# Performance work log

Hardware: AMD Instinct MI355X
Metric: run time of the kernel (lower is better)

Reference implementation:

```python
import jax, jax.numpy as jnp
import numpy as np

EPS = 1e-8  # PoissonNLLLoss default eps

def _pair_loss(inp, tgt):
    # Poisson NLL (log_input=False, full=True), summed over detector dim D,
    # for every (hypothesis i, measurement j) pair WITHOUT materializing [N,M,D]:
    # loss_ij = sum_d inp[i,d] - sum_d tgt[j,d]*log(inp[i,d]+eps) + sum_d stirling(tgt[j,d])
    log_in = jnp.log(inp + EPS)                         # [N,D]
    s_in = jnp.sum(inp, axis=1)                         # [N]
    cross = jnp.einsum('id,jd->ij', log_in, tgt)        # [N,M]
    t_safe = jnp.where(tgt > 1, tgt, 1.0)
    stirling = jnp.where(
        tgt > 1,
        tgt * jnp.log(t_safe) - tgt + 0.5 * jnp.log(2.0 * jnp.pi * t_safe),
        0.0,
    )
    s_st = jnp.sum(stirling, axis=1)                    # [M]
    return s_in[:, None] - cross + s_st[None, :]        # [N,M]

def setup_inputs() -> dict:
    key = jax.random.key(0)
    k1, k2 = jax.random.split(key)
    N, M, D = 10000, 10000, 180
    # photon-count-like positive values; scale so target>1 hits Stirling branch
    inp = jax.random.uniform(k1, (N, D), dtype=jnp.float32) * 100.0
    tgt = jax.random.uniform(k2, (M, D), dtype=jnp.float32) * 100.0
    return {"input": inp, "target": tgt}

def reference(input, target):
    L = _pair_loss(input, target)          # [N,M]
    loss_v = jnp.min(L, axis=1)            # [N]
    match = jnp.argmin(L, axis=1)          # [N] int
    loss = jnp.mean(loss_v)
    return (loss, match)
```

## Files before the change

### kernel.cpp

```cpp
#include <hip/hip_runtime.h>
#include <math.h>

#define EPSF 1e-8f

typedef _Float16 f16x8 __attribute__((ext_vector_type(8)));
typedef float f32x4 __attribute__((ext_vector_type(4)));

#define GLOAD_LDS16(g, l)                                                      \
  __builtin_amdgcn_global_load_lds(                                            \
      (const __attribute__((address_space(1))) unsigned int*)(g),              \
      (__attribute__((address_space(3))) unsigned int*)(l), 16, 0, 0)

#define WAITV(n) asm volatile("s_waitcnt vmcnt(" #n ")" ::: "memory")
#define BAR() __builtin_amdgcn_s_barrier()

__device__ __forceinline__ unsigned int ord_from_float(float f) {
  unsigned int u = __float_as_uint(f);
  return (u & 0x80000000u) ? ~u : (u | 0x80000000u);
}

__device__ __forceinline__ float float_from_ord(unsigned int o) {
  return (o & 0x80000000u) ? __uint_as_float(o & 0x7fffffffu)
                           : __uint_as_float(~o);
}

__device__ __forceinline__ unsigned long long shfl_xor_u64(unsigned long long x, int m) {
  int lo = __shfl_xor((int)(unsigned int)(x & 0xffffffffull), m, 64);
  int hi = __shfl_xor((int)(unsigned int)(x >> 32), m, 64);
  return ((unsigned long long)(unsigned int)hi << 32) | (unsigned int)lo;
}

__global__ __launch_bounds__(64) void prep_A_kernel(
    const float* __restrict__ inp, _Float16* __restrict__ Acat,
    float* __restrict__ s_in, unsigned long long* __restrict__ packed,
    int N, int D, int DP) {
  int r = blockIdx.x;
  const size_t base = (size_t)r * (3 * DP);
  float s = 0.f;
  for (int d = threadIdx.x; d < DP; d += 64) {
    float lg = 0.f;
    if (r < N && d < D) {
      float x = inp[(size_t)r * D + d];
      s += x;
      lg = logf(x + EPSF);
    }
    _Float16 h = (_Float16)lg;
    _Float16 l = (_Float16)(lg - (float)h);
    Acat[base + d] = h;
    Acat[base + DP + d] = h;
    Acat[base + 2 * DP + d] = l;
  }
  #pragma unroll
  for (int m = 1; m < 64; m <<= 1) s += __shfl_xor(s, m, 64);
  if (threadIdx.x == 0 && r < N) {
    s_in[r] = s;
    packed[r] = ~0ull;
  }
}

__global__ __launch_bounds__(64) void prep_B_kernel(
    const float* __restrict__ tgt, _Float16* __restrict__ Bcat,
    float* __restrict__ s_st, int M, int D, int DP) {
  int r = blockIdx.x;
  const size_t base = (size_t)r * (3 * DP);
  float s = 0.f;
  for (int d = threadIdx.x; d < DP; d += 64) {
    float x = 0.f;
    if (r < M && d < D) {
      x = tgt[(size_t)r * D + d];
      if (x > 1.0f)
        s += x * logf(x) - x + 0.5f * logf(6.283185307179586f * x);
    }
    _Float16 h = (_Float16)x;
    _Float16 l = (_Float16)(x - (float)h);
    Bcat[base + d] = h;
    Bcat[base + DP + d] = l;
    Bcat[base + 2 * DP + d] = h;
  }
  #pragma unroll
  for (int m = 1; m < 64; m <<= 1) s += __shfl_xor(s, m, 64);
  if (threadIdx.x == 0 && r < M) s_st[r] = s;
}

#define BT 256
#define BUFH 8192

__global__ __launch_bounds__(512, 2) void mfma_pair_min_kernel(
    const _Float16* __restrict__ Acat, const _Float16* __restrict__ Bcat,
    const float* __restrict__ s_st, unsigned long long* __restrict__ packed,
    int N, int M, int KP, int gx) {
  extern __shared__ __align__(16) _Float16 smem[];
  _Float16* const AshB = smem;
  _Float16* const BshB = smem + 4 * BUFH;

  const int t = threadIdx.x;
  const int lane = t & 63;
  const int wid = t >> 6;
  const int wr = wid >> 2;
  const int wc = wid & 3;

  const int nwg = gridDim.x;
  const int q8 = nwg >> 3;
  const int xcd = blockIdx.x & 7;
  const int i8 = blockIdx.x >> 3;
  int brow, bcol;
  if (q8 % gx == 0) {
    int bh = q8 / gx;
    brow = xcd * bh + i8 % bh;
    bcol = i8 / bh;
  } else {
    int wg = xcd * q8 + i8;
    brow = wg / gx;
    bcol = wg % gx;
  }
  const int row0 = brow * BT;
  const int col0 = bcol * BT;

  f32x4 acc[8][4] = {};

  const int srow = lane >> 2;
  const int gs = (lane & 3) ^ ((lane >> 3) & 3);
  const _Float16* const aSrc = Acat + (size_t)(row0 + wid * 32 + srow) * KP + gs * 8;
  const _Float16* const bSrc = Bcat + (size_t)(col0 + wid * 32 + srow) * KP + gs * 8;
  _Float16* const lA = AshB + wid * 1024;
  _Float16* const lB = BshB + wid * 1024;

#define STAGE(buf, step)                                                       \
  do {                                                                         \
    const int so_ = (step) * 32;                                               \
    GLOAD_LDS16(aSrc + so_, lA + (buf) * BUFH);                                \
    GLOAD_LDS16(aSrc + so_ + 16 * KP, lA + (buf) * BUFH + 512);                \
    GLOAD_LDS16(bSrc + so_, lB + (buf) * BUFH);                                \
    GLOAD_LDS16(bSrc + so_ + 16 * KP, lB + (buf) * BUFH + 512);                \
  } while (0)

  const int rl = lane & 15;
  const int qq = lane >> 4;
  const int sa = qq ^ ((rl >> 1) & 3);

#define COMPUTE(buf)                                                           \
  do {                                                                         \
    const int bofs_ = (buf) * BUFH;                                            \
    f16x8 af[8], bf[4];                                                        \
    _Pragma("unroll")                                                          \
    for (int m = 0; m < 8; ++m)                                                \
      af[m] = *(const f16x8*)(&AshB[bofs_ + (wr * 128 + m * 16 + rl) * 32 + sa * 8]); \
    _Pragma("unroll")                                                          \
    for (int n = 0; n < 4; ++n)                                                \
      bf[n] = *(const f16x8*)(&BshB[bofs_ + (wc * 64 + n * 16 + rl) * 32 + sa * 8]); \
    __builtin_amdgcn_s_setprio(1);                                             \
    _Pragma("unroll")                                                          \
    for (int m = 0; m < 8; ++m)                                                \
      _Pragma("unroll")                                                        \
      for (int n = 0; n < 4; ++n)                                              \
        acc[m][n] = __builtin_amdgcn_mfma_f32_16x16x32_f16(af[m], bf[n],       \
                                                           acc[m][n], 0, 0, 0); \
    __builtin_amdgcn_s_setprio(0);                                             \
  } while (0)

  const int NT = KP >> 5;

  STAGE(0, 0);
  STAGE(1, 1);
  STAGE(2, 2);
  WAITV(8);
  BAR();

  int kt = 0;
  for (; kt < NT - 3; ++kt) {
    STAGE((kt + 3) & 3, kt + 3);
    COMPUTE(kt & 3);
    WAITV(8);
    BAR();
  }
  COMPUTE(kt & 3);
  WAITV(4);
  BAR();
  ++kt;
  COMPUTE(kt & 3);
  WAITV(0);
  BAR();
  ++kt;
  COMPUTE(kt & 3);

#undef STAGE
#undef COMPUTE

  float stv[4];
  #pragma unroll
  for (int n = 0; n < 4; ++n) {
    int gj = col0 + wc * 64 + n * 16 + rl;
    stv[n] = (gj < M) ? s_st[gj] : __builtin_inff();
  }
  #pragma unroll
  for (int m = 0; m < 8; ++m) {
    #pragma unroll
    for (int g = 0; g < 4; ++g) {
      int grow = row0 + wr * 128 + m * 16 + qq * 4 + g;
      unsigned long long bst = ~0ull;
      #pragma unroll
      for (int n = 0; n < 4; ++n) {
        int gj = col0 + wc * 64 + n * 16 + rl;
        float val = stv[n] - acc[m][n][g];
        unsigned long long p =
            ((unsigned long long)ord_from_float(val) << 32) | (unsigned int)gj;
        if (p < bst) bst = p;
      }
      #pragma unroll
      for (int mm = 1; mm < 16; mm <<= 1) {
        unsigned long long o = shfl_xor_u64(bst, mm);
        if (o < bst) bst = o;
      }
      if (rl == 0 && grow < N) atomicMin(&packed[grow], bst);
    }
  }
}


__global__ __launch_bounds__(256) void finalize_kernel(
    const unsigned long long* __restrict__ packed,
    const float* __restrict__ s_in, float* __restrict__ out, int N) {
  __shared__ double sh[256];
  double s = 0.0;
  for (int i = threadIdx.x; i < N; i += 256) {
    unsigned long long p = packed[i];
    float val = float_from_ord((unsigned int)(p >> 32));
    out[1 + i] = (float)(unsigned int)(p & 0xffffffffull);
    s += (double)(s_in[i] + val);
  }
  sh[threadIdx.x] = s;
  __syncthreads();
  for (int off = 128; off > 0; off >>= 1) {
    if (threadIdx.x < off) sh[threadIdx.x] += sh[threadIdx.x + off];
    __syncthreads();
  }
  if (threadIdx.x == 0) out[0] = (float)(sh[0] / N);
}

extern "C" void kernel_launch(void* const* d_in, const int* in_sizes, int n_in,
                              void* d_out, int out_size, void* d_ws, size_t ws_size,
                              hipStream_t stream) {
  const float* inp = (const float*)d_in[0];
  const float* tgt = (const float*)d_in[1];
  float* out = (float*)d_out;

  int N = out_size - 1;
  int D = in_sizes[0] / N;
  int M = in_sizes[1] / D;

  int Npad = ((N + BT - 1) / BT) * BT;
  int Mpad = ((M + BT - 1) / BT) * BT;
  int DP = ((D + 31) / 32) * 32;
  int KP = 3 * DP;

  char* ws = (char*)d_ws;
  size_t off = 0;
  float* s_in = (float*)(ws + off); off += (size_t)N * 4;
  float* s_st = (float*)(ws + off); off += (size_t)M * 4;
  off = (off + 15) & ~(size_t)15;
  unsigned long long* packed = (unsigned long long*)(ws + off); off += (size_t)N * 8;
  off = (off + 15) & ~(size_t)15;
  _Float16* Acat = (_Float16*)(ws + off); off += (size_t)Npad * KP * 2;
  _Float16* Bcat = (_Float16*)(ws + off); off += (size_t)Mpad * KP * 2;

  prep_A_kernel<<<Npad, 64, 0, stream>>>(inp, Acat, s_in, packed, N, D, DP);
  prep_B_kernel<<<Mpad, 64, 0, stream>>>(tgt, Bcat, s_st, M, D, DP);

  const int ldsBytes = 8 * BUFH * 2;
  hipFuncSetAttribute((const void*)mfma_pair_min_kernel,
                      hipFuncAttributeMaxDynamicSharedMemorySize, ldsBytes);

  int gx = Mpad / BT, gy = Npad / BT;
  mfma_pair_min_kernel<<<gx * gy, 512, ldsBytes, stream>>>(Acat, Bcat, s_st,
                                                           packed, N, M, KP, gx);

  finalize_kernel<<<1, 256, 0, stream>>>(packed, s_in, out, N);
}
```

Before: 213.7 us.

## Restructure MFMA main loop into ping-pong register-fragment pipeline over 64-wide K tiles

Rewrites the GEMM main loop so each 64-wide K tile is split into two K halves and two M halves. LDS fragment loads for the next quarter-tile are interleaved with the MFMAs of the current one through double-buffered register fragments, and global-to-LDS stages are spread across the sub-steps. The K dimension is padded to an odd number of 64-element tiles, with zero fill in the prep kernels, to fit the unrolled two-tile loop. This is meant to hide LDS read latency behind MFMA work, at the cost of more barriers per tile, a few extra padded K elements, and a fragile hand-written schedule.

```diff
diff --git a/kernel.cpp b/kernel.cpp
--- a/kernel.cpp
+++ b/kernel.cpp
@@ -33,9 +33,9 @@
 __global__ __launch_bounds__(64) void prep_A_kernel(
     const float* __restrict__ inp, _Float16* __restrict__ Acat,
     float* __restrict__ s_in, unsigned long long* __restrict__ packed,
-    int N, int D, int DP) {
+    int N, int D, int DP, int KPA) {
   int r = blockIdx.x;
-  const size_t base = (size_t)r * (3 * DP);
+  _Float16* row = Acat + (size_t)r * KPA;
   float s = 0.f;
   for (int d = threadIdx.x; d < DP; d += 64) {
     float lg = 0.f;
@@ -46,10 +46,11 @@
     }
     _Float16 h = (_Float16)lg;
     _Float16 l = (_Float16)(lg - (float)h);
-    Acat[base + d] = h;
-    Acat[base + DP + d] = h;
-    Acat[base + 2 * DP + d] = l;
-  }
+    row[d] = h;
+    row[DP + d] = h;
+    row[2 * DP + d] = l;
+  }
+  for (int d = threadIdx.x; d < KPA - 3 * DP; d += 64) row[3 * DP + d] = (_Float16)0.f;
   #pragma unroll
   for (int m = 1; m < 64; m <<= 1) s += __shfl_xor(s, m, 64);
   if (threadIdx.x == 0 && r < N) {
@@ -60,9 +61,9 @@
 
 __global__ __launch_bounds__(64) void prep_B_kernel(
     const float* __restrict__ tgt, _Float16* __restrict__ Bcat,
-    float* __restrict__ s_st, int M, int D, int DP) {
+    float* __restrict__ s_st, int M, int D, int DP, int KPA) {
   int r = blockIdx.x;
-  const size_t base = (size_t)r * (3 * DP);
+  _Float16* row = Bcat + (size_t)r * KPA;
   float s = 0.f;
   for (int d = threadIdx.x; d < DP; d += 64) {
     float x = 0.f;
@@ -73,26 +74,24 @@
     }
     _Float16 h = (_Float16)x;
     _Float16 l = (_Float16)(x - (float)h);
-    Bcat[base + d] = h;
-    Bcat[base + DP + d] = l;
-    Bcat[base + 2 * DP + d] = h;
-  }
+    row[d] = h;
+    row[DP + d] = l;
+    row[2 * DP + d] = h;
+  }
+  for (int d = threadIdx.x; d < KPA - 3 * DP; d += 64) row[3 * DP + d] = (_Float16)0.f;
   #pragma unroll
   for (int m = 1; m < 64; m <<= 1) s += __shfl_xor(s, m, 64);
   if (threadIdx.x == 0 && r < M) s_st[r] = s;
 }
 
 #define BT 256
-#define BUFH 8192
+#define UNITH 8192
 
 __global__ __launch_bounds__(512, 2) void mfma_pair_min_kernel(
     const _Float16* __restrict__ Acat, const _Float16* __restrict__ Bcat,
     const float* __restrict__ s_st, unsigned long long* __restrict__ packed,
-    int N, int M, int KP, int gx) {
+    int N, int M, int KPA, int gx) {
   extern __shared__ __align__(16) _Float16 smem[];
-  _Float16* const AshB = smem;
-  _Float16* const BshB = smem + 4 * BUFH;
-
   const int t = threadIdx.x;
   const int lane = t & 63;
   const int wid = t >> 6;
@@ -116,75 +115,92 @@
   const int row0 = brow * BT;
   const int col0 = bcol * BT;
 
-  f32x4 acc[8][4] = {};
-
   const int srow = lane >> 2;
   const int gs = (lane & 3) ^ ((lane >> 3) & 3);
-  const _Float16* const aSrc = Acat + (size_t)(row0 + wid * 32 + srow) * KP + gs * 8;
-  const _Float16* const bSrc = Bcat + (size_t)(col0 + wid * 32 + srow) * KP + gs * 8;
-  _Float16* const lA = AshB + wid * 1024;
-  _Float16* const lB = BshB + wid * 1024;
-
-#define STAGE(buf, step)                                                       \
-  do {                                                                         \
-    const int so_ = (step) * 32;                                               \
-    GLOAD_LDS16(aSrc + so_, lA + (buf) * BUFH);                                \
-    GLOAD_LDS16(aSrc + so_ + 16 * KP, lA + (buf) * BUFH + 512);                \
-    GLOAD_LDS16(bSrc + so_, lB + (buf) * BUFH);                                \
-    GLOAD_LDS16(bSrc + so_ + 16 * KP, lB + (buf) * BUFH + 512);                \
+  const _Float16* pA0 = Acat + (size_t)(row0 + wid * 32 + srow) * KPA + gs * 8;
+  const _Float16* pA1 = pA0 + (size_t)16 * KPA;
+  const _Float16* pB0 = Bcat + (size_t)(col0 + wid * 32 + srow) * KPA + gs * 8;
+  const _Float16* pB1 = pB0 + (size_t)16 * KPA;
+  _Float16* const ldst = smem + wid * 1024;
+
+#define STG(b_, isB_, kh_, tofs_)                                              \
+  do {                                                                         \
+    const _Float16* s0_ = ((isB_) ? pB0 : pA0) + (tofs_) * 64 + (kh_) * 32;    \
+    const _Float16* s1_ = ((isB_) ? pB1 : pA1) + (tofs_) * 64 + (kh_) * 32;    \
+    _Float16* d_ = ldst + ((((b_) << 2) | ((isB_) << 1) | (kh_)) * UNITH);     \
+    GLOAD_LDS16(s0_, d_);                                                      \
+    GLOAD_LDS16(s1_, d_ + 512);                                                \
   } while (0)
 
   const int rl = lane & 15;
-  const int qq = lane >> 4;
-  const int sa = qq ^ ((rl >> 1) & 3);
-
-#define COMPUTE(buf)                                                           \
-  do {                                                                         \
-    const int bofs_ = (buf) * BUFH;                                            \
-    f16x8 af[8], bf[4];                                                        \
-    _Pragma("unroll")                                                          \
-    for (int m = 0; m < 8; ++m)                                                \
-      af[m] = *(const f16x8*)(&AshB[bofs_ + (wr * 128 + m * 16 + rl) * 32 + sa * 8]); \
-    _Pragma("unroll")                                                          \
-    for (int n = 0; n < 4; ++n)                                                \
-      bf[n] = *(const f16x8*)(&BshB[bofs_ + (wc * 64 + n * 16 + rl) * 32 + sa * 8]); \
+  const int q = lane >> 4;
+  const int sa = q ^ ((rl >> 1) & 3);
+
+#define LDA4(dst_, b_, kh_, mh_)                                               \
+  do {                                                                         \
+    const _Float16* p_ = smem + ((((b_) << 2) | (kh_)) * UNITH);               \
+    _Pragma("unroll") for (int mm_ = 0; mm_ < 4; ++mm_)                        \
+        dst_[mm_] = *(const f16x8*)(p_ + (wr * 128 + (mh_) * 64 + mm_ * 16 + rl) * 32 + sa * 8); \
+  } while (0)
+
+#define LDB4(dst_, b_, kh_)                                                    \
+  do {                                                                         \
+    const _Float16* p_ = smem + ((((b_) << 2) | 2 | (kh_)) * UNITH);           \
+    _Pragma("unroll") for (int nn_ = 0; nn_ < 4; ++nn_)                        \
+        dst_[nn_] = *(const f16x8*)(p_ + (wc * 64 + nn_ * 16 + rl) * 32 + sa * 8); \
+  } while (0)
+
+  f32x4 acc[8][4] = {};
+  f16x8 afA[4], afB[4], bfA[4], bfB[4];
+
+#define MMQ(af_, bf_, mh_)                                                     \
+  do {                                                                         \
     __builtin_amdgcn_s_setprio(1);                                             \
-    _Pragma("unroll")                                                          \
-    for (int m = 0; m < 8; ++m)                                                \
-      _Pragma("unroll")                                                        \
-      for (int n = 0; n < 4; ++n)                                              \
-        acc[m][n] = __builtin_amdgcn_mfma_f32_16x16x32_f16(af[m], bf[n],       \
-                                                           acc[m][n], 0, 0, 0); \
+    _Pragma("unroll") for (int mm_ = 0; mm_ < 4; ++mm_)                        \
+        _Pragma("unroll") for (int nn_ = 0; nn_ < 4; ++nn_)                    \
+            acc[(mh_) * 4 + mm_][nn_] = __builtin_amdgcn_mfma_f32_16x16x32_f16(\
+                af_[mm_], bf_[nn_], acc[(mh_) * 4 + mm_][nn_], 0, 0, 0);       \
     __builtin_amdgcn_s_setprio(0);                                             \
   } while (0)
 
-  const int NT = KP >> 5;
-
-  STAGE(0, 0);
-  STAGE(1, 1);
-  STAGE(2, 2);
-  WAITV(8);
+  STG(0, 0, 0, 0); STG(0, 1, 0, 0); STG(0, 0, 1, 0); STG(0, 1, 1, 0);
+  STG(1, 0, 0, 1); STG(1, 1, 0, 1); STG(1, 1, 1, 1);
+  WAITV(10);
   BAR();
-
-  int kt = 0;
-  for (; kt < NT - 3; ++kt) {
-    STAGE((kt + 3) & 3, kt + 3);
-    COMPUTE(kt & 3);
-    WAITV(8);
-    BAR();
-  }
-  COMPUTE(kt & 3);
-  WAITV(4);
-  BAR();
-  ++kt;
-  COMPUTE(kt & 3);
-  WAITV(0);
-  BAR();
-  ++kt;
-  COMPUTE(kt & 3);
-
-#undef STAGE
-#undef COMPUTE
+  LDA4(afA, 0, 0, 0);
+  LDB4(bfA, 0, 0);
+
+  const int LITERS = ((KPA >> 6) - 3) >> 1;
+  for (int i = 0; i < LITERS; ++i) {
+    LDA4(afB, 0, 0, 1); STG(1, 0, 1, 1);                  BAR(); MMQ(afA, bfA, 0); WAITV(8); BAR();
+    LDA4(afA, 0, 1, 0); LDB4(bfB, 0, 1); STG(0, 0, 0, 2); BAR(); MMQ(afB, bfA, 1);           BAR();
+    LDA4(afB, 0, 1, 1); STG(0, 1, 0, 2);                  BAR(); MMQ(afA, bfB, 0); WAITV(8); BAR();
+    LDA4(afA, 1, 0, 0); LDB4(bfA, 1, 0); STG(0, 1, 1, 2); BAR(); MMQ(afB, bfB, 1);           BAR();
+    LDA4(afB, 1, 0, 1); STG(0, 0, 1, 2);                  BAR(); MMQ(afA, bfA, 0); WAITV(8); BAR();
+    LDA4(afA, 1, 1, 0); LDB4(bfB, 1, 1); STG(1, 1, 0, 3); BAR(); MMQ(afB, bfA, 1);           BAR();
+    LDA4(afB, 1, 1, 1); STG(1, 0, 0, 3);                  BAR(); MMQ(afA, bfB, 0); WAITV(8); BAR();
+    LDA4(afA, 0, 0, 0); LDB4(bfA, 0, 0); STG(1, 1, 1, 3); BAR(); MMQ(afB, bfB, 1);           BAR();
+    pA0 += 128; pA1 += 128; pB0 += 128; pB1 += 128;
+  }
+
+  LDA4(afB, 0, 0, 1); STG(1, 0, 1, 1);                  BAR(); MMQ(afA, bfA, 0); WAITV(8); BAR();
+  LDA4(afA, 0, 1, 0); LDB4(bfB, 0, 1); STG(0, 0, 0, 2); BAR(); MMQ(afB, bfA, 1);           BAR();
+  LDA4(afB, 0, 1, 1); STG(0, 1, 0, 2);                  BAR(); MMQ(afA, bfB, 0); WAITV(8); BAR();
+  LDA4(afA, 1, 0, 0); LDB4(bfA, 1, 0); STG(0, 1, 1, 2); BAR(); MMQ(afB, bfB, 1);           BAR();
+  LDA4(afB, 1, 0, 1); STG(0, 0, 1, 2);                  BAR(); MMQ(afA, bfA, 0); WAITV(8); BAR();
+  LDA4(afA, 1, 1, 0); LDB4(bfB, 1, 1);                  BAR(); MMQ(afB, bfA, 1);           BAR();
+  LDA4(afB, 1, 1, 1);                                   BAR(); MMQ(afA, bfB, 0); WAITV(4); BAR();
+  LDA4(afA, 0, 0, 0); LDB4(bfA, 0, 0);                  BAR(); MMQ(afB, bfB, 1);           BAR();
+
+  LDA4(afB, 0, 0, 1);                                   BAR(); MMQ(afA, bfA, 0); WAITV(0); BAR();
+  LDA4(afA, 0, 1, 0); LDB4(bfB, 0, 1);                  BAR(); MMQ(afB, bfA, 1);           BAR();
+  LDA4(afB, 0, 1, 1);                                   BAR(); MMQ(afA, bfB, 0);           BAR();
+                                                        BAR(); MMQ(afB, bfB, 1);
+
+#undef STG
+#undef LDA4
+#undef LDB4
+#undef MMQ
 
   float stv[4];
   #pragma unroll
@@ -196,7 +212,7 @@
   for (int m = 0; m < 8; ++m) {
     #pragma unroll
     for (int g = 0; g < 4; ++g) {
-      int grow = row0 + wr * 128 + m * 16 + qq * 4 + g;
+      int grow = row0 + wr * 128 + m * 16 + q * 4 + g;
       unsigned long long bst = ~0ull;
       #pragma unroll
       for (int n = 0; n < 4; ++n) {
@@ -251,7 +267,9 @@
   int Npad = ((N + BT - 1) / BT) * BT;
   int Mpad = ((M + BT - 1) / BT) * BT;
   int DP = ((D + 31) / 32) * 32;
-  int KP = 3 * DP;
+  int TT = (3 * DP + 63) / 64;
+  if ((TT & 1) == 0) ++TT;
+  int KPA = TT * 64;
 
   char* ws = (char*)d_ws;
   size_t off = 0;
@@ -260,19 +278,19 @@
   off = (off + 15) & ~(size_t)15;
   unsigned long long* packed = (unsigned long long*)(ws + off); off += (size_t)N * 8;
   off = (off + 15) & ~(size_t)15;
-  _Float16* Acat = (_Float16*)(ws + off); off += (size_t)Npad * KP * 2;
-  _Float16* Bcat = (_Float16*)(ws + off); off += (size_t)Mpad * KP * 2;
-
-  prep_A_kernel<<<Npad, 64, 0, stream>>>(inp, Acat, s_in, packed, N, D, DP);
-  prep_B_kernel<<<Mpad, 64, 0, stream>>>(tgt, Bcat, s_st, M, D, DP);
-
-  const int ldsBytes = 8 * BUFH * 2;
+  _Float16* Acat = (_Float16*)(ws + off); off += (size_t)Npad * KPA * 2;
+  _Float16* Bcat = (_Float16*)(ws + off); off += (size_t)Mpad * KPA * 2;
+
+  prep_A_kernel<<<Npad, 64, 0, stream>>>(inp, Acat, s_in, packed, N, D, DP, KPA);
+  prep_B_kernel<<<Mpad, 64, 0, stream>>>(tgt, Bcat, s_st, M, D, DP, KPA);
+
+  const int ldsBytes = 8 * UNITH * 2;
   hipFuncSetAttribute((const void*)mfma_pair_min_kernel,
                       hipFuncAttributeMaxDynamicSharedMemorySize, ldsBytes);
 
   int gx = Mpad / BT, gy = Npad / BT;
   mfma_pair_min_kernel<<<gx * gy, 512, ldsBytes, stream>>>(Acat, Bcat, s_st,
-                                                           packed, N, M, KP, gx);
+                                                           packed, N, M, KPA, gx);
 
   finalize_kernel<<<1, 256, 0, stream>>>(packed, s_in, out, N);
 }
```

After: 213.1 us. No clear change (-0.3%).

## Replace global atomicMin with per-tile partial minima and parallel reduction

Applied to the files above, without the earlier changes.

The main kernel now reduces the row minima across its four column-warps in shared memory and writes one partial result per (column tile, row) to a buffer, instead of issuing global 64-bit atomicMin calls. A new multi-block reduce kernel takes the min over column tiles and accumulates the mean through a fixed-point atomic add. This replaces the single-block finalize. The two prep kernels are merged into one launch. The trade is an extra partial buffer plus two extra small launches and a memset, in exchange for removing atomic contention and the serial finalize.

```diff
diff --git a/kernel.cpp b/kernel.cpp
--- a/kernel.cpp
+++ b/kernel.cpp
@@ -30,56 +30,52 @@
   return ((unsigned long long)(unsigned int)hi << 32) | (unsigned int)lo;
 }
 
-__global__ __launch_bounds__(64) void prep_A_kernel(
-    const float* __restrict__ inp, _Float16* __restrict__ Acat,
-    float* __restrict__ s_in, unsigned long long* __restrict__ packed,
-    int N, int D, int DP) {
-  int r = blockIdx.x;
-  const size_t base = (size_t)r * (3 * DP);
-  float s = 0.f;
-  for (int d = threadIdx.x; d < DP; d += 64) {
-    float lg = 0.f;
-    if (r < N && d < D) {
-      float x = inp[(size_t)r * D + d];
-      s += x;
-      lg = logf(x + EPSF);
-    }
-    _Float16 h = (_Float16)lg;
-    _Float16 l = (_Float16)(lg - (float)h);
-    Acat[base + d] = h;
-    Acat[base + DP + d] = h;
-    Acat[base + 2 * DP + d] = l;
-  }
-  #pragma unroll
-  for (int m = 1; m < 64; m <<= 1) s += __shfl_xor(s, m, 64);
-  if (threadIdx.x == 0 && r < N) {
-    s_in[r] = s;
-    packed[r] = ~0ull;
-  }
-}
-
-__global__ __launch_bounds__(64) void prep_B_kernel(
-    const float* __restrict__ tgt, _Float16* __restrict__ Bcat,
-    float* __restrict__ s_st, int M, int D, int DP) {
-  int r = blockIdx.x;
-  const size_t base = (size_t)r * (3 * DP);
-  float s = 0.f;
-  for (int d = threadIdx.x; d < DP; d += 64) {
-    float x = 0.f;
-    if (r < M && d < D) {
-      x = tgt[(size_t)r * D + d];
-      if (x > 1.0f)
-        s += x * logf(x) - x + 0.5f * logf(6.283185307179586f * x);
-    }
-    _Float16 h = (_Float16)x;
-    _Float16 l = (_Float16)(x - (float)h);
-    Bcat[base + d] = h;
-    Bcat[base + DP + d] = l;
-    Bcat[base + 2 * DP + d] = h;
-  }
-  #pragma unroll
-  for (int m = 1; m < 64; m <<= 1) s += __shfl_xor(s, m, 64);
-  if (threadIdx.x == 0 && r < M) s_st[r] = s;
+__global__ __launch_bounds__(64) void prep_kernel(
+    const float* __restrict__ inp, const float* __restrict__ tgt,
+    _Float16* __restrict__ Acat, _Float16* __restrict__ Bcat,
+    float* __restrict__ s_in, float* __restrict__ s_st,
+    int N, int M, int Npad, int Mpad, int D, int DP, int KPA) {
+  const int r = blockIdx.x;
+  if (r < Npad) {
+    _Float16* row = Acat + (size_t)r * KPA;
+    float s = 0.f;
+    for (int d = threadIdx.x; d < DP; d += 64) {
+      float lg = 0.f;
+      if (r < N && d < D) {
+        float x = inp[(size_t)r * D + d];
+        s += x;
+        lg = logf(x + EPSF);
+      }
+      _Float16 h = (_Float16)lg;
+      _Float16 l = (_Float16)(lg - (float)h);
+      row[d] = h;
+      row[DP + d] = h;
+      row[2 * DP + d] = l;
+    }
+    #pragma unroll
+    for (int m = 1; m < 64; m <<= 1) s += __shfl_xor(s, m, 64);
+    if (threadIdx.x == 0 && r < N) s_in[r] = s;
+  }
+  if (r < Mpad) {
+    _Float16* row = Bcat + (size_t)r * KPA;
+    float s = 0.f;
+    for (int d = threadIdx.x; d < DP; d += 64) {
+      float x = 0.f;
+      if (r < M && d < D) {
+        x = tgt[(size_t)r * D + d];
+        if (x > 1.0f)
+          s += x * logf(x) - x + 0.5f * logf(6.283185307179586f * x);
+      }
+      _Float16 h = (_Float16)x;
+      _Float16 l = (_Float16)(x - (float)h);
+      row[d] = h;
+      row[DP + d] = l;
+      row[2 * DP + d] = h;
+    }
+    #pragma unroll
+    for (int m = 1; m < 64; m <<= 1) s += __shfl_xor(s, m, 64);
+    if (threadIdx.x == 0 && r < M) s_st[r] = s;
+  }
 }
 
 #define BT 256
@@ -87,8 +83,8 @@
 
 __global__ __launch_bounds__(512, 2) void mfma_pair_min_kernel(
     const _Float16* __restrict__ Acat, const _Float16* __restrict__ Bcat,
-    const float* __restrict__ s_st, unsigned long long* __restrict__ packed,
-    int N, int M, int KP, int gx) {
+    const float* __restrict__ s_st, unsigned long long* __restrict__ packed2,
+    int N, int M, int KPA, int gx, int Npad) {
   extern __shared__ __align__(16) _Float16 smem[];
   _Float16* const AshB = smem;
   _Float16* const BshB = smem + 4 * BUFH;
@@ -120,18 +116,18 @@
 
   const int srow = lane >> 2;
   const int gs = (lane & 3) ^ ((lane >> 3) & 3);
-  const _Float16* const aSrc = Acat + (size_t)(row0 + wid * 32 + srow) * KP + gs * 8;
-  const _Float16* const bSrc = Bcat + (size_t)(col0 + wid * 32 + srow) * KP + gs * 8;
-  _Float16* const lA = AshB + wid * 1024;
-  _Float16* const lB = BshB + wid * 1024;
+  const _Float16* a0 = Acat + (size_t)(row0 + wid * 32 + srow) * KPA + gs * 8;
+  const _Float16* a1 = a0 + (size_t)16 * KPA;
+  const _Float16* b0 = Bcat + (size_t)(col0 + wid * 32 + srow) * KPA + gs * 8;
+  const _Float16* b1 = b0 + (size_t)16 * KPA;
 
 #define STAGE(buf, step)                                                       \
   do {                                                                         \
     const int so_ = (step) * 32;                                               \
-    GLOAD_LDS16(aSrc + so_, lA + (buf) * BUFH);                                \
-    GLOAD_LDS16(aSrc + so_ + 16 * KP, lA + (buf) * BUFH + 512);                \
-    GLOAD_LDS16(bSrc + so_, lB + (buf) * BUFH);                                \
-    GLOAD_LDS16(bSrc + so_ + 16 * KP, lB + (buf) * BUFH + 512);                \
+    GLOAD_LDS16(a0 + so_, AshB + wid * 1024 + (buf) * BUFH);                   \
+    GLOAD_LDS16(a1 + so_, AshB + wid * 1024 + (buf) * BUFH + 512);             \
+    GLOAD_LDS16(b0 + so_, BshB + wid * 1024 + (buf) * BUFH);                   \
+    GLOAD_LDS16(b1 + so_, BshB + wid * 1024 + (buf) * BUFH + 512);             \
   } while (0)
 
   const int rl = lane & 15;
@@ -158,7 +154,7 @@
     __builtin_amdgcn_s_setprio(0);                                             \
   } while (0)
 
-  const int NT = KP >> 5;
+  const int NT = KPA >> 5;
 
   STAGE(0, 0);
   STAGE(1, 1);
@@ -192,11 +188,14 @@
     int gj = col0 + wc * 64 + n * 16 + rl;
     stv[n] = (gj < M) ? s_st[gj] : __builtin_inff();
   }
+
+  __syncthreads();
+  unsigned long long* red = (unsigned long long*)smem;
+
   #pragma unroll
   for (int m = 0; m < 8; ++m) {
     #pragma unroll
     for (int g = 0; g < 4; ++g) {
-      int grow = row0 + wr * 128 + m * 16 + qq * 4 + g;
       unsigned long long bst = ~0ull;
       #pragma unroll
       for (int n = 0; n < 4; ++n) {
@@ -211,30 +210,60 @@
         unsigned long long o = shfl_xor_u64(bst, mm);
         if (o < bst) bst = o;
       }
-      if (rl == 0 && grow < N) atomicMin(&packed[grow], bst);
-    }
-  }
-}
-
-
-__global__ __launch_bounds__(256) void finalize_kernel(
-    const unsigned long long* __restrict__ packed,
-    const float* __restrict__ s_in, float* __restrict__ out, int N) {
+      if (rl == 0)
+        red[wc * 256 + wr * 128 + m * 16 + qq * 4 + g] = bst;
+    }
+  }
+  __syncthreads();
+
+  if (t < 256) {
+    int grow = row0 + t;
+    if (grow < N) {
+      unsigned long long b0 = red[t];
+      unsigned long long b1 = red[256 + t];
+      unsigned long long b2 = red[512 + t];
+      unsigned long long b3 = red[768 + t];
+      unsigned long long best = b0 < b1 ? b0 : b1;
+      if (b2 < best) best = b2;
+      if (b3 < best) best = b3;
+      packed2[(size_t)bcol * Npad + grow] = best;
+    }
+  }
+}
+
+__global__ __launch_bounds__(256) void reduce_kernel(
+    const unsigned long long* __restrict__ packed2,
+    const float* __restrict__ s_in, float* __restrict__ out,
+    unsigned long long* __restrict__ sumbuf, int N, int Npad, int gx) {
+  int i = blockIdx.x * 256 + threadIdx.x;
+  double local = 0.0;
+  if (i < N) {
+    unsigned long long best = ~0ull;
+    for (int c = 0; c < gx; ++c) {
+      unsigned long long p = packed2[(size_t)c * Npad + i];
+      if (p < best) best = p;
+    }
+    out[1 + i] = (float)(unsigned int)(best & 0xffffffffull);
+    float val = float_from_ord((unsigned int)(best >> 32));
+    local = (double)(s_in[i] + val);
+  }
   __shared__ double sh[256];
-  double s = 0.0;
-  for (int i = threadIdx.x; i < N; i += 256) {
-    unsigned long long p = packed[i];
-    float val = float_from_ord((unsigned int)(p >> 32));
-    out[1 + i] = (float)(unsigned int)(p & 0xffffffffull);
-    s += (double)(s_in[i] + val);
-  }
-  sh[threadIdx.x] = s;
+  sh[threadIdx.x] = local;
   __syncthreads();
-  for (int off = 128; off > 0; off >>= 1) {
-    if (threadIdx.x < off) sh[threadIdx.x] += sh[threadIdx.x + off];
+  for (int o = 128; o > 0; o >>= 1) {
+    if (threadIdx.x < o) sh[threadIdx.x] += sh[threadIdx.x + o];
     __syncthreads();
   }
-  if (threadIdx.x == 0) out[0] = (float)(sh[0] / N);
+  if (threadIdx.x == 0) {
+    long long q = __double2ll_rn(sh[0] * 1048576.0);
+    atomicAdd(sumbuf, (unsigned long long)q);
+  }
+}
+
+__global__ void final_kernel(const unsigned long long* __restrict__ sumbuf,
+                             float* __restrict__ out, int N) {
+  if (threadIdx.x == 0)
+    out[0] = (float)(((double)(long long)sumbuf[0] / 1048576.0) / (double)N);
 }
 
 extern "C" void kernel_launch(void* const* d_in, const int* in_sizes, int n_in,
@@ -251,28 +280,33 @@
   int Npad = ((N + BT - 1) / BT) * BT;
   int Mpad = ((M + BT - 1) / BT) * BT;
   int DP = ((D + 31) / 32) * 32;
-  int KP = 3 * DP;
+  int KPA = ((3 * DP + 31) / 32) * 32;
+  int gx = Mpad / BT, gy = Npad / BT;
 
   char* ws = (char*)d_ws;
   size_t off = 0;
   float* s_in = (float*)(ws + off); off += (size_t)N * 4;
   float* s_st = (float*)(ws + off); off += (size_t)M * 4;
   off = (off + 15) & ~(size_t)15;
-  unsigned long long* packed = (unsigned long long*)(ws + off); off += (size_t)N * 8;
-  off = (off + 15) & ~(size_t)15;
-  _Float16* Acat = (_Float16*)(ws + off); off += (size_t)Npad * KP * 2;
-  _Float16* Bcat = (_Float16*)(ws + off); off += (size_t)Mpad * KP * 2;
-
-  prep_A_kernel<<<Npad, 64, 0, stream>>>(inp, Acat, s_in, packed, N, D, DP);
-  prep_B_kernel<<<Mpad, 64, 0, stream>>>(tgt, Bcat, s_st, M, D, DP);
+  unsigned long long* sumbuf = (unsigned long long*)(ws + off); off += 16;
+  unsigned long long* packed2 = (unsigned long long*)(ws + off);
+  off += (size_t)gx * Npad * 8;
+  _Float16* Acat = (_Float16*)(ws + off); off += (size_t)Npad * KPA * 2;
+  _Float16* Bcat = (_Float16*)(ws + off); off += (size_t)Mpad * KPA * 2;
+
+  hipMemsetAsync(sumbuf, 0, 8, stream);
+
+  int pgrid = Npad > Mpad ? Npad : Mpad;
+  prep_kernel<<<pgrid, 64, 0, stream>>>(inp, tgt, Acat, Bcat, s_in, s_st,
+                                        N, M, Npad, Mpad, D, DP, KPA);
 
   const int ldsBytes = 8 * BUFH * 2;
   hipFuncSetAttribute((const void*)mfma_pair_min_kernel,
                       hipFuncAttributeMaxDynamicSharedMemorySize, ldsBytes);
-
-  int gx = Mpad / BT, gy = Npad / BT;
-  mfma_pair_min_kernel<<<gx * gy, 512, ldsBytes, stream>>>(Acat, Bcat, s_st,
-                                                           packed, N, M, KP, gx);
-
-  finalize_kernel<<<1, 256, 0, stream>>>(packed, s_in, out, N);
-}
+  mfma_pair_min_kernel<<<gx * gy, 512, ldsBytes, stream>>>(
+      Acat, Bcat, s_st, packed2, N, M, KPA, gx, Npad);
+
+  reduce_kernel<<<(N + 255) / 256, 256, 0, stream>>>(packed2, s_in, out,
+                                                     sumbuf, N, Npad, gx);
+  final_kernel<<<1, 64, 0, stream>>>(sumbuf, out, N);
+}
```

After: 225.6 us. 5.6% more time.
